# Optimization experiments

Hardware: AMD Instinct MI355X
Metric: run time of the kernel (lower is better)

## Reference

```python
import jax, jax.numpy as jnp
import numpy as np

N = 65536            # query points (256x256 image)
G = 2048             # number of gaussian/gabor primitives
K = 8                # top-k wave frequencies per primitive
NUM_TOTAL_FREQ = 128
MAX_FREQ = 128.0


def setup_inputs() -> dict:
    key = jax.random.key(0)
    ks = jax.random.split(key, 7)
    x = jax.random.uniform(ks[0], (N, 2), jnp.float32)
    gaussian_colors = 0.05 * jax.random.normal(ks[1], (G, 3), jnp.float32)
    gaussian_positions = jax.random.uniform(ks[2], (G, 2), jnp.float32)
    gaussian_scales = 3.0 + 0.05 * jax.random.normal(ks[3], (G, 2), jnp.float32)
    gaussian_rotations = jnp.pi * jax.random.uniform(ks[4], (G, 1), jnp.float32)
    topk_wave_coefficients = 0.01 * (2.0 * jax.random.uniform(ks[5], (G, K), jnp.float32) - 1.0)
    topk_wave_indices = jax.random.randint(ks[6], (G, K), 0, NUM_TOTAL_FREQ)
    return {
        "x": x,
        "gaussian_colors": gaussian_colors,
        "gaussian_positions": gaussian_positions,
        "gaussian_scales": gaussian_scales,
        "gaussian_rotations": gaussian_rotations,
        "topk_wave_coefficients": topk_wave_coefficients,
        "topk_wave_indices": topk_wave_indices,
    }


def reference(x, gaussian_colors, gaussian_positions, gaussian_scales,
              gaussian_rotations, topk_wave_coefficients, topk_wave_indices):
    # Dense (unblocked) faithful evaluation of the periodic-primitive splat:
    # out[n] = sum_g color_g * exp(-0.5*((rx*sx)^2+(ry*sy)^2)) * sum_k c_gk*cos(2*pi*f_gk*rx)
    dx = x[:, None, 0] - gaussian_positions[None, :, 0]   # [N, G]
    dy = x[:, None, 1] - gaussian_positions[None, :, 1]   # [N, G]
    th = gaussian_rotations[:, 0]                          # [G]
    c, s = jnp.cos(th), jnp.sin(th)
    rx = c[None, :] * dx + s[None, :] * dy                 # rotated coords [N, G]
    ry = -s[None, :] * dx + c[None, :] * dy
    sx = gaussian_scales[None, :, 0]
    sy = gaussian_scales[None, :, 1]
    env = jnp.exp(-0.5 * ((rx * sx) ** 2 + (ry * sy) ** 2))  # gaussian envelope [N, G]
    # frequency of each selected coefficient: idx * max_freq / num_total_freq
    freqs = topk_wave_indices.astype(jnp.float32) * (MAX_FREQ / NUM_TOTAL_FREQ)  # [G, K]
    two_pi = 2.0 * jnp.pi
    wave = jnp.zeros_like(env)
    for k in range(K):  # small fixed loop -> avoids materializing [N, G, K]
        wave = wave + topk_wave_coefficients[:, k][None, :] * jnp.cos(two_pi * freqs[:, k][None, :] * rx)
    return (env * wave) @ gaussian_colors  # [N, 3]
```

## Files before the change

kernel.cpp:

```cpp
#include <hip/hip_runtime.h>
#include <math.h>

#define G_NUM   2048
#define N_PTS   65536
#define K_FREQ  8
#define REC     64
#define CHUNKS  32
#define G_PER_CHUNK (G_NUM / CHUNKS)
#define PACK_BYTES ((size_t)G_NUM * REC * sizeof(float))
#define PART_FLOATS ((size_t)N_PTS * 3)
#define PART_BYTES_OLD (PART_FLOATS * sizeof(float) * CHUNKS)
#define LDS_FLOATS  (G_PER_CHUNK * REC)

#define S_TAB   2048
#define INV_H   (2048.0f / 3.0f)
#define TAB_BYTES   ((size_t)G_NUM * S_TAB * 16)
#define XS_BYTES    ((size_t)N_PTS * 8)
#define PERM_BYTES  ((size_t)N_PTS * 4)
#define PART4_BYTES ((size_t)CHUNKS * N_PTS * 16)
#define HIST_BYTES  ((size_t)1024 * 4)
#define OFF_TAB   (PACK_BYTES)
#define OFF_XS    (OFF_TAB + TAB_BYTES)
#define OFF_PERM  (OFF_XS + XS_BYTES)
#define OFF_PART4 (OFF_PERM + PERM_BYTES)
#define OFF_HIST  (OFF_PART4 + PART4_BYTES)
#define NEW_TOTAL (OFF_HIST + HIST_BYTES)

typedef float v2f __attribute__((ext_vector_type(2)));

#if __has_builtin(__builtin_amdgcn_cosf)
__device__ __forceinline__ float hw_cos_rev(float p) { return __builtin_amdgcn_cosf(p); }
#else
__device__ __forceinline__ float hw_cos_rev(float p) { return __cosf(6.28318530717958648f * p); }
#endif
#if __has_builtin(__builtin_amdgcn_exp2f)
__device__ __forceinline__ float hw_exp2(float p) { return __builtin_amdgcn_exp2f(p); }
#else
__device__ __forceinline__ float hw_exp2(float p) { return exp2f(p); }
#endif
#if __has_builtin(__builtin_amdgcn_fractf)
__device__ __forceinline__ float hw_fract(float p) { return __builtin_amdgcn_fractf(p); }
#else
__device__ __forceinline__ float hw_fract(float p) { return p - floorf(p); }
#endif

__device__ __forceinline__ v2f fma2v(v2f a, v2f b, v2f c) {
#if __has_builtin(__builtin_elementwise_fma)
    return __builtin_elementwise_fma(a, b, c);
#else
    v2f r; r.x = fmaf(a.x, b.x, c.x); r.y = fmaf(a.y, b.y, c.y); return r;
#endif
}

__global__ __launch_bounds__(256) void pack_kernel(
    const float* __restrict__ colors, const float* __restrict__ pos,
    const float* __restrict__ scales, const float* __restrict__ rot,
    const float* __restrict__ coef,   const int* __restrict__ idx,
    float* __restrict__ pack)
{
    int j = blockIdx.x * blockDim.x + threadIdx.x;
    if (j >= G_NUM) return;
    float th = rot[j];
    float c = cosf(th), s = sinf(th);
    float px = pos[2 * j], py = pos[2 * j + 1];
    float sx = scales[2 * j], sy = scales[2 * j + 1];
    const float nhl2e = -0.72134752044448170368f;
    float* r = pack + (size_t)j * REC;
    auto put = [&](int pair, float v) { r[2 * pair] = v; r[2 * pair + 1] = v; };
    put(0, -(c * px + s * py));
    put(1, s * px - c * py);
    put(2, c);
    put(3, s);
    put(4, -s);
    put(5, nhl2e * sx * sx);
    put(6, nhl2e * sy * sy);
    put(7, colors[3 * j]);
    put(8, colors[3 * j + 1]);
    put(9, colors[3 * j + 2]);
#pragma unroll
    for (int k = 0; k < K_FREQ; ++k) {
        put(10 + k, (float)idx[j * K_FREQ + k]);
        put(18 + k, coef[j * K_FREQ + k]);
    }
#pragma unroll
    for (int p = 26; p < 32; ++p) put(p, 0.0f);
}

template <bool USE_PART>
__global__ __launch_bounds__(256, 8) void periodic2d_kernel(
    const float* __restrict__ x, const float* __restrict__ pack,
    float* __restrict__ dst)
{
    __shared__ float lds_rec[LDS_FLOATS];
    {
        const float4* __restrict__ src = (const float4*)
            (pack + (size_t)(blockIdx.y * G_PER_CHUNK) * REC);
        float4* dstl = (float4*)lds_rec;
#pragma unroll
        for (int i = 0; i < LDS_FLOATS / 4 / 256; ++i)
            dstl[threadIdx.x + 256 * i] = src[threadIdx.x + 256 * i];
    }
    __syncthreads();

    const int t = blockIdx.x * 256 + threadIdx.x;
    const int p0 = t;
    const int p1 = t + N_PTS / 4;
    const int p2 = t + N_PTS / 2;
    const int p3 = t + 3 * (N_PTS / 4);
    const float2 q0 = ((const float2*)x)[p0];
    const float2 q1 = ((const float2*)x)[p1];
    const float2 q2 = ((const float2*)x)[p2];
    const float2 q3 = ((const float2*)x)[p3];
    const v2f xiA = {q0.x, q1.x}, yiA = {q0.y, q1.y};
    const v2f xiB = {q2.x, q3.x}, yiB = {q2.y, q3.y};
    v2f a0A = {0.f, 0.f}, a1A = {0.f, 0.f}, a2A = {0.f, 0.f};
    v2f a0B = {0.f, 0.f}, a1B = {0.f, 0.f}, a2B = {0.f, 0.f};

    const v2f* rv = (const v2f*)lds_rec;
#pragma unroll 1
    for (int j = 0; j < G_PER_CHUNK; ++j, rv += REC / 2) {
        const v2f rxA = fma2v(xiA, rv[2], fma2v(yiA, rv[3], rv[0]));
        const v2f rxB = fma2v(xiB, rv[2], fma2v(yiB, rv[3], rv[0]));
        const v2f ryA = fma2v(yiA, rv[2], fma2v(xiA, rv[4], rv[1]));
        const v2f ryB = fma2v(yiB, rv[2], fma2v(xiB, rv[4], rv[1]));
        const v2f eargA = fma2v(ryA * rv[6], ryA, (rxA * rv[5]) * rxA);
        const v2f eargB = fma2v(ryB * rv[6], ryB, (rxB * rv[5]) * rxB);
        v2f envA, envB;
        envA.x = hw_exp2(eargA.x); envA.y = hw_exp2(eargA.y);
        envB.x = hw_exp2(eargB.x); envB.y = hw_exp2(eargB.y);
        v2f waveA = {0.f, 0.f}, waveB = {0.f, 0.f};
#pragma unroll
        for (int k = 0; k < K_FREQ; ++k) {
            const v2f phA = rxA * rv[10 + k];
            const v2f phB = rxB * rv[10 + k];
            v2f cA, cB;
            cA.x = hw_cos_rev(phA.x); cA.y = hw_cos_rev(phA.y);
            cB.x = hw_cos_rev(phB.x); cB.y = hw_cos_rev(phB.y);
            waveA = fma2v(cA, rv[18 + k], waveA);
            waveB = fma2v(cB, rv[18 + k], waveB);
        }
        const v2f wA = envA * waveA;
        const v2f wB = envB * waveB;
        a0A = fma2v(wA, rv[7], a0A);  a0B = fma2v(wB, rv[7], a0B);
        a1A = fma2v(wA, rv[8], a1A);  a1B = fma2v(wB, rv[8], a1B);
        a2A = fma2v(wA, rv[9], a2A);  a2B = fma2v(wB, rv[9], a2B);
    }

    if (USE_PART) {
        float* o = dst + (size_t)blockIdx.y * PART_FLOATS;
        o[3 * p0 + 0] = a0A.x; o[3 * p0 + 1] = a1A.x; o[3 * p0 + 2] = a2A.x;
        o[3 * p1 + 0] = a0A.y; o[3 * p1 + 1] = a1A.y; o[3 * p1 + 2] = a2A.y;
        o[3 * p2 + 0] = a0B.x; o[3 * p2 + 1] = a1B.x; o[3 * p2 + 2] = a2B.x;
        o[3 * p3 + 0] = a0B.y; o[3 * p3 + 1] = a1B.y; o[3 * p3 + 2] = a2B.y;
    } else {
        atomicAdd(&dst[3 * p0 + 0], a0A.x);
        atomicAdd(&dst[3 * p0 + 1], a1A.x);
        atomicAdd(&dst[3 * p0 + 2], a2A.x);
        atomicAdd(&dst[3 * p1 + 0], a0A.y);
        atomicAdd(&dst[3 * p1 + 1], a1A.y);
        atomicAdd(&dst[3 * p1 + 2], a2A.y);
        atomicAdd(&dst[3 * p2 + 0], a0B.x);
        atomicAdd(&dst[3 * p2 + 1], a1B.x);
        atomicAdd(&dst[3 * p2 + 2], a2B.x);
        atomicAdd(&dst[3 * p3 + 0], a0B.y);
        atomicAdd(&dst[3 * p3 + 1], a1B.y);
        atomicAdd(&dst[3 * p3 + 2], a2B.y);
    }
}

__global__ __launch_bounds__(256) void reduce_kernel(
    const float* __restrict__ part, float* __restrict__ out)
{
    const int i = blockIdx.x * 256 + threadIdx.x;
    float4 s = {0.f, 0.f, 0.f, 0.f};
#pragma unroll
    for (int c = 0; c < CHUNKS; ++c) {
        const float4 v = ((const float4*)(part + (size_t)c * PART_FLOATS))[i];
        s.x += v.x; s.y += v.y; s.z += v.z; s.w += v.w;
    }
    ((float4*)out)[i] = s;
}


__global__ __launch_bounds__(256) void build_tab_kernel(
    const float* __restrict__ colors, const float* __restrict__ pos,
    const float* __restrict__ scales, const float* __restrict__ rot,
    const float* __restrict__ coef,   const int* __restrict__ idx,
    float* __restrict__ pack, float* __restrict__ tab)
{
    const int g = blockIdx.y;
    if (blockIdx.x == 0 && threadIdx.x == 0) {
        float th = rot[g];
        float c = cosf(th), s = sinf(th);
        float px = pos[2 * g], py = pos[2 * g + 1];
        float sx = scales[2 * g], sy = scales[2 * g + 1];
        const float nhl2e = -0.72134752044448170368f;
        float* r = pack + (size_t)g * REC;
        auto put = [&](int pair, float v) { r[2 * pair] = v; r[2 * pair + 1] = v; };
        put(0, -(c * px + s * py));
        put(1, s * px - c * py);
        put(2, c); put(3, s); put(4, -s);
        put(5, nhl2e * sx * sx);
        put(6, nhl2e * sy * sy);
        put(7, colors[3 * g]); put(8, colors[3 * g + 1]); put(9, colors[3 * g + 2]);
    }
    const int i = blockIdx.x * 256 + threadIdx.x;
    float nk[K_FREQ], ck[K_FREQ];
#pragma unroll
    for (int k = 0; k < K_FREQ; ++k) {
        nk[k] = (float)idx[g * K_FREQ + k];
        ck[k] = coef[g * K_FREQ + k];
    }
    float w[4];
#pragma unroll
    for (int m = 0; m < 4; ++m) {
        const float xm = (float)(3 * i + m - 3072) * 0x1p-11f;
        float acc = 0.f;
#pragma unroll
        for (int k = 0; k < K_FREQ; ++k)
            acc = fmaf(ck[k], hw_cos_rev(nk[k] * xm), acc);
        w[m] = acc;
    }
    const float d1 = w[1] - w[0];
    const float d2 = w[2] - 2.f * w[1] + w[0];
    const float d3 = w[3] - 3.f * w[2] + 3.f * w[1] - w[0];
    float4 o;
    o.x = w[0];
    o.y = 3.f * d1 - 1.5f * d2 + d3;
    o.z = 4.5f * (d2 - d3);
    o.w = 4.5f * d3;
    ((float4*)tab)[(size_t)g * S_TAB + i] = o;
}

__device__ __forceinline__ int cell_id(float px, float py) {
    int cx = (int)(px * 32.f); cx = cx > 31 ? 31 : cx;
    int cy = (int)(py * 32.f); cy = cy > 31 ? 31 : cy;
    int m = 0;
#pragma unroll
    for (int b = 0; b < 5; ++b)
        m |= (((cx >> b) & 1) << (2 * b)) | (((cy >> b) & 1) << (2 * b + 1));
    return m;
}

__global__ __launch_bounds__(256) void hist_kernel(
    const float* __restrict__ x, int* __restrict__ hist)
{
    __shared__ int h[1024];
#pragma unroll
    for (int i = 0; i < 4; ++i) h[threadIdx.x + 256 * i] = 0;
    __syncthreads();
    const int t = blockIdx.x * 256 + threadIdx.x;
    const float4 p = ((const float4*)x)[t];
    atomicAdd(&h[cell_id(p.x, p.y)], 1);
    atomicAdd(&h[cell_id(p.z, p.w)], 1);
    __syncthreads();
#pragma unroll
    for (int i = 0; i < 4; ++i) {
        const int b = threadIdx.x + 256 * i;
        const int v = h[b];
        if (v) atomicAdd(&hist[b], v);
    }
}

__global__ __launch_bounds__(1024) void scan_kernel(int* __restrict__ hist)
{
    __shared__ int e[1024];
    const int tid = threadIdx.x;
    const int v = hist[tid];
    e[tid] = v;
    __syncthreads();
#pragma unroll 1
    for (int d = 1; d < 1024; d <<= 1) {
        const int a = (tid >= d) ? e[tid - d] : 0;
        __syncthreads();
        e[tid] += a;
        __syncthreads();
    }
    hist[tid] = e[tid] - v;
}

__global__ __launch_bounds__(256) void scatter_kernel(
    const float* __restrict__ x, int* __restrict__ cursor,
    float* __restrict__ xs, int* __restrict__ perm)
{
    const int t = blockIdx.x * 256 + threadIdx.x;
    const float4 p = ((const float4*)x)[t];
    const int i0 = 2 * t;
    int pos = atomicAdd(&cursor[cell_id(p.x, p.y)], 1);
    ((float2*)xs)[pos] = make_float2(p.x, p.y);
    perm[pos] = i0;
    pos = atomicAdd(&cursor[cell_id(p.z, p.w)], 1);
    ((float2*)xs)[pos] = make_float2(p.z, p.w);
    perm[pos] = i0 + 1;
}

struct PipeSet {
    v2f envA, envB, tfA, tfB;
    float4 cA0, cA1, cB0, cB1;
    v2f col0, col1, col2;
};

__global__ __launch_bounds__(256, 4) void periodic2d_tab_kernel(
    const float* __restrict__ xs, const float* __restrict__ pack,
    const float* __restrict__ tab, float* __restrict__ part)
{
    __shared__ float lds_rec[G_PER_CHUNK * 32];
    {
        const float4* __restrict__ src = (const float4*)
            (pack + (size_t)(blockIdx.y * G_PER_CHUNK) * REC);
        float4* d4 = (float4*)lds_rec;
#pragma unroll
        for (int it = 0; it < 2; ++it) {
            const int i = threadIdx.x + 256 * it;
            d4[i] = src[((i >> 3) << 4) | (i & 7)];
        }
    }
    __syncthreads();

    const int t = blockIdx.x * 256 + threadIdx.x;
    const int p0 = ((t >> 6) << 8) | (t & 63);
    const float2 q0 = ((const float2*)xs)[p0];
    const float2 q1 = ((const float2*)xs)[p0 + 64];
    const float2 q2 = ((const float2*)xs)[p0 + 128];
    const float2 q3 = ((const float2*)xs)[p0 + 192];
    const v2f xiA = {q0.x, q1.x}, yiA = {q0.y, q1.y};
    const v2f xiB = {q2.x, q3.x}, yiB = {q2.y, q3.y};
    v2f a0A = {0.f, 0.f}, a1A = {0.f, 0.f}, a2A = {0.f, 0.f};
    v2f a0B = {0.f, 0.f}, a1B = {0.f, 0.f}, a2B = {0.f, 0.f};
    const v2f vinvh = {INV_H, INV_H};
    const v2f voff  = {1024.f, 1024.f};

    const v2f* __restrict__ rv = (const v2f*)lds_rec;
    const float4* __restrict__ tb =
        (const float4*)tab + (size_t)(blockIdx.y * G_PER_CHUNK) * S_TAB;

    PipeSet s0, s1;

    auto ISSUE = [&](PipeSet& S, const v2f* __restrict__ r,
                     const float4* __restrict__ tbl) {
        const v2f rxA = fma2v(xiA, r[2], fma2v(yiA, r[3], r[0]));
        const v2f rxB = fma2v(xiB, r[2], fma2v(yiB, r[3], r[0]));
        const v2f ryA = fma2v(yiA, r[2], fma2v(xiA, r[4], r[1]));
        const v2f ryB = fma2v(yiB, r[2], fma2v(xiB, r[4], r[1]));
        const v2f eargA = fma2v(ryA * r[6], ryA, (rxA * r[5]) * rxA);
        const v2f eargB = fma2v(ryB * r[6], ryB, (rxB * r[5]) * rxB);
        S.envA.x = hw_exp2(eargA.x); S.envA.y = hw_exp2(eargA.y);
        S.envB.x = hw_exp2(eargB.x); S.envB.y = hw_exp2(eargB.y);
        const v2f uA = fma2v(rxA, vinvh, voff);
        const v2f uB = fma2v(rxB, vinvh, voff);
        const int iA0 = (int)uA.x, iA1 = (int)uA.y;
        const int iB0 = (int)uB.x, iB1 = (int)uB.y;
        S.tfA.x = hw_fract(uA.x); S.tfA.y = hw_fract(uA.y);
        S.tfB.x = hw_fract(uB.x); S.tfB.y = hw_fract(uB.y);
        S.cA0 = tbl[iA0]; S.cA1 = tbl[iA1];
        S.cB0 = tbl[iB0]; S.cB1 = tbl[iB1];
        S.col0 = r[7]; S.col1 = r[8]; S.col2 = r[9];
    };

    auto CONSUME = [&](PipeSet& S) {
        v2f wvA, wvB;
        wvA.x = fmaf(fmaf(fmaf(S.cA0.w, S.tfA.x, S.cA0.z), S.tfA.x, S.cA0.y), S.tfA.x, S.cA0.x);
        wvA.y = fmaf(fmaf(fmaf(S.cA1.w, S.tfA.y, S.cA1.z), S.tfA.y, S.cA1.y), S.tfA.y, S.cA1.x);
        wvB.x = fmaf(fmaf(fmaf(S.cB0.w, S.tfB.x, S.cB0.z), S.tfB.x, S.cB0.y), S.tfB.x, S.cB0.x);
        wvB.y = fmaf(fmaf(fmaf(S.cB1.w, S.tfB.y, S.cB1.z), S.tfB.y, S.cB1.y), S.tfB.y, S.cB1.x);
        const v2f wA = S.envA * wvA;
        const v2f wB = S.envB * wvB;
        a0A = fma2v(wA, S.col0, a0A);  a0B = fma2v(wB, S.col0, a0B);
        a1A = fma2v(wA, S.col1, a1A);  a1B = fma2v(wB, S.col1, a1B);
        a2A = fma2v(wA, S.col2, a2A);  a2B = fma2v(wB, S.col2, a2B);
    };

    ISSUE(s0, rv,      tb);
    ISSUE(s1, rv + 16, tb + S_TAB);
#pragma unroll 1
    for (int j = 0; j < G_PER_CHUNK - 2; j += 2) {
        CONSUME(s0);
        ISSUE(s0, rv + 16 * (j + 2), tb + (size_t)S_TAB * (j + 2));
        CONSUME(s1);
        ISSUE(s1, rv + 16 * (j + 3), tb + (size_t)S_TAB * (j + 3));
    }
    CONSUME(s0);
    CONSUME(s1);

    float4* o = (float4*)part + (size_t)blockIdx.y * N_PTS;
    o[p0      ] = make_float4(a0A.x, a1A.x, a2A.x, 0.f);
    o[p0 +  64] = make_float4(a0A.y, a1A.y, a2A.y, 0.f);
    o[p0 + 128] = make_float4(a0B.x, a1B.x, a2B.x, 0.f);
    o[p0 + 192] = make_float4(a0B.y, a1B.y, a2B.y, 0.f);
}

__global__ __launch_bounds__(256) void reduce_tab_kernel(
    const float* __restrict__ part, const int* __restrict__ perm,
    float* __restrict__ out)
{
    const int p = blockIdx.x * 256 + threadIdx.x;
    const float4* p4 = (const float4*)part;
    float sx = 0.f, sy = 0.f, sz = 0.f;
#pragma unroll
    for (int c = 0; c < CHUNKS; ++c) {
        const float4 v = p4[(size_t)c * N_PTS + p];
        sx += v.x; sy += v.y; sz += v.z;
    }
    const int q = perm[p];
    out[3 * q    ] = sx;
    out[3 * q + 1] = sy;
    out[3 * q + 2] = sz;
}

extern "C" void kernel_launch(void* const* d_in, const int* in_sizes, int n_in,
                              void* d_out, int out_size, void* d_ws, size_t ws_size,
                              hipStream_t stream)
{
    const float* x      = (const float*)d_in[0];
    const float* colors = (const float*)d_in[1];
    const float* pos    = (const float*)d_in[2];
    const float* scales = (const float*)d_in[3];
    const float* rot    = (const float*)d_in[4];
    const float* coef   = (const float*)d_in[5];
    const int*   idx    = (const int*)d_in[6];
    float* out  = (float*)d_out;
    float* pack = (float*)d_ws;

    if (ws_size >= NEW_TOTAL) {
        float* tab  = (float*)((char*)d_ws + OFF_TAB);
        float* xs   = (float*)((char*)d_ws + OFF_XS);
        int*   perm = (int*)  ((char*)d_ws + OFF_PERM);
        float* part = (float*)((char*)d_ws + OFF_PART4);
        int*   hist = (int*)  ((char*)d_ws + OFF_HIST);
        (void)hipMemsetAsync(hist, 0, HIST_BYTES, stream);
        build_tab_kernel<<<dim3(S_TAB / 256, G_NUM), 256, 0, stream>>>(
            colors, pos, scales, rot, coef, idx, pack, tab);
        hist_kernel<<<dim3(N_PTS / 512), 256, 0, stream>>>(x, hist);
        scan_kernel<<<dim3(1), 1024, 0, stream>>>(hist);
        scatter_kernel<<<dim3(N_PTS / 512), 256, 0, stream>>>(x, hist, xs, perm);
        periodic2d_tab_kernel<<<dim3(N_PTS / 1024, CHUNKS), 256, 0, stream>>>(
            xs, pack, tab, part);
        reduce_tab_kernel<<<dim3(N_PTS / 256), 256, 0, stream>>>(part, perm, out);
        return;
    }

    float* part = (float*)((char*)d_ws + PACK_BYTES);
    pack_kernel<<<dim3((G_NUM + 255) / 256), 256, 0, stream>>>(
        colors, pos, scales, rot, coef, idx, pack);
    if (ws_size >= PACK_BYTES + PART_BYTES_OLD) {
        periodic2d_kernel<true><<<dim3(N_PTS / 1024, CHUNKS), 256, 0, stream>>>(
            x, pack, part);
        reduce_kernel<<<dim3((N_PTS * 3 / 4) / 256), 256, 0, stream>>>(part, out);
    } else {
        (void)hipMemsetAsync(d_out, 0, (size_t)out_size * sizeof(float), stream);
        periodic2d_kernel<false><<<dim3(N_PTS / 1024, CHUNKS), 256, 0, stream>>>(
            x, pack, out);
    }
}
```

Measured before the change: 204.2 us.

## Fuse table build with per-block histograms and drop memset and scan kernels

```diff
diff --git a/kernel.cpp b/kernel.cpp
--- a/kernel.cpp
+++ b/kernel.cpp
@@ -5,7 +5,7 @@
 #define N_PTS   65536
 #define K_FREQ  8
 #define REC     64
-#define CHUNKS  32
+#define CHUNKS  16
 #define G_PER_CHUNK (G_NUM / CHUNKS)
 #define PACK_BYTES ((size_t)G_NUM * REC * sizeof(float))
 #define PART_FLOATS ((size_t)N_PTS * 3)
@@ -14,17 +14,19 @@
 
 #define S_TAB   2048
 #define INV_H   (2048.0f / 3.0f)
+#define TAB_BLOCKS  (G_NUM * (S_TAB / 256))
+#define HIST_BLOCKS 64
 #define TAB_BYTES   ((size_t)G_NUM * S_TAB * 16)
 #define XS_BYTES    ((size_t)N_PTS * 8)
 #define PERM_BYTES  ((size_t)N_PTS * 4)
 #define PART4_BYTES ((size_t)CHUNKS * N_PTS * 16)
-#define HIST_BYTES  ((size_t)1024 * 4)
+#define PHIST_BYTES ((size_t)HIST_BLOCKS * 1024 * 4)
 #define OFF_TAB   (PACK_BYTES)
 #define OFF_XS    (OFF_TAB + TAB_BYTES)
 #define OFF_PERM  (OFF_XS + XS_BYTES)
 #define OFF_PART4 (OFF_PERM + PERM_BYTES)
-#define OFF_HIST  (OFF_PART4 + PART4_BYTES)
-#define NEW_TOTAL (OFF_HIST + HIST_BYTES)
+#define OFF_PHIST (OFF_PART4 + PART4_BYTES)
+#define NEW_TOTAL (OFF_PHIST + PHIST_BYTES)
 
 typedef float v2f __attribute__((ext_vector_type(2)));
 
@@ -182,14 +184,48 @@
 }
 
 
-__global__ __launch_bounds__(256) void build_tab_kernel(
+__device__ __forceinline__ int cell_id(float px, float py) {
+    int cx = (int)(px * 32.f); cx = cx > 31 ? 31 : cx;
+    int cy = (int)(py * 32.f); cy = cy > 31 ? 31 : cy;
+    int m = 0;
+#pragma unroll
+    for (int b = 0; b < 5; ++b)
+        m |= (((cx >> b) & 1) << (2 * b)) | (((cy >> b) & 1) << (2 * b + 1));
+    return m;
+}
+
+__global__ __launch_bounds__(256) void build_hist_kernel(
     const float* __restrict__ colors, const float* __restrict__ pos,
     const float* __restrict__ scales, const float* __restrict__ rot,
     const float* __restrict__ coef,   const int* __restrict__ idx,
-    float* __restrict__ pack, float* __restrict__ tab)
-{
-    const int g = blockIdx.y;
-    if (blockIdx.x == 0 && threadIdx.x == 0) {
+    const float* __restrict__ x,
+    float* __restrict__ pack, float* __restrict__ tab,
+    int* __restrict__ phist)
+{
+    __shared__ int h[1024];
+    const int b = blockIdx.x;
+    if (b >= TAB_BLOCKS) {
+        const int r = b - TAB_BLOCKS;
+#pragma unroll
+        for (int i = 0; i < 4; ++i) h[threadIdx.x + 256 * i] = 0;
+        __syncthreads();
+        const float4* xv = (const float4*)x + (size_t)r * 512;
+#pragma unroll
+        for (int it = 0; it < 2; ++it) {
+            const float4 p = xv[threadIdx.x + 256 * it];
+            atomicAdd(&h[cell_id(p.x, p.y)], 1);
+            atomicAdd(&h[cell_id(p.z, p.w)], 1);
+        }
+        __syncthreads();
+        int* row = phist + r * 1024;
+#pragma unroll
+        for (int i = 0; i < 4; ++i)
+            row[threadIdx.x + 256 * i] = h[threadIdx.x + 256 * i];
+        return;
+    }
+    const int g  = b >> 3;
+    const int bx = b & 7;
+    if (bx == 0 && threadIdx.x == 0) {
         float th = rot[g];
         float c = cosf(th), s = sinf(th);
         float px = pos[2 * g], py = pos[2 * g + 1];
@@ -204,7 +240,7 @@
         put(6, nhl2e * sy * sy);
         put(7, colors[3 * g]); put(8, colors[3 * g + 1]); put(9, colors[3 * g + 2]);
     }
-    const int i = blockIdx.x * 256 + threadIdx.x;
+    const int i = bx * 256 + threadIdx.x;
     float nk[K_FREQ], ck[K_FREQ];
 #pragma unroll
     for (int k = 0; k < K_FREQ; ++k) {
@@ -232,66 +268,50 @@
     ((float4*)tab)[(size_t)g * S_TAB + i] = o;
 }
 
-__device__ __forceinline__ int cell_id(float px, float py) {
-    int cx = (int)(px * 32.f); cx = cx > 31 ? 31 : cx;
-    int cy = (int)(py * 32.f); cy = cy > 31 ? 31 : cy;
-    int m = 0;
-#pragma unroll
-    for (int b = 0; b < 5; ++b)
-        m |= (((cx >> b) & 1) << (2 * b)) | (((cy >> b) & 1) << (2 * b + 1));
-    return m;
-}
-
-__global__ __launch_bounds__(256) void hist_kernel(
-    const float* __restrict__ x, int* __restrict__ hist)
-{
-    __shared__ int h[1024];
-#pragma unroll
-    for (int i = 0; i < 4; ++i) h[threadIdx.x + 256 * i] = 0;
-    __syncthreads();
-    const int t = blockIdx.x * 256 + threadIdx.x;
-    const float4 p = ((const float4*)x)[t];
-    atomicAdd(&h[cell_id(p.x, p.y)], 1);
-    atomicAdd(&h[cell_id(p.z, p.w)], 1);
-    __syncthreads();
-#pragma unroll
-    for (int i = 0; i < 4; ++i) {
-        const int b = threadIdx.x + 256 * i;
-        const int v = h[b];
-        if (v) atomicAdd(&hist[b], v);
-    }
-}
-
-__global__ __launch_bounds__(1024) void scan_kernel(int* __restrict__ hist)
-{
-    __shared__ int e[1024];
-    const int tid = threadIdx.x;
-    const int v = hist[tid];
-    e[tid] = v;
+__global__ __launch_bounds__(256) void scatter_kernel(
+    const float* __restrict__ x, const int* __restrict__ phist,
+    float* __restrict__ xs, int* __restrict__ perm)
+{
+    __shared__ int e[256];
+    __shared__ int cur[1024];
+    const int r = blockIdx.x;
+    const int t = threadIdx.x;
+    int4 tot = {0, 0, 0, 0}, base = {0, 0, 0, 0};
+#pragma unroll 1
+    for (int rr = 0; rr < HIST_BLOCKS; ++rr) {
+        const int4 v = ((const int4*)(phist + rr * 1024))[t];
+        if (rr < r) { base.x += v.x; base.y += v.y; base.z += v.z; base.w += v.w; }
+        tot.x += v.x; tot.y += v.y; tot.z += v.z; tot.w += v.w;
+    }
+    const int s4 = tot.x + tot.y + tot.z + tot.w;
+    e[t] = s4;
     __syncthreads();
 #pragma unroll 1
-    for (int d = 1; d < 1024; d <<= 1) {
-        const int a = (tid >= d) ? e[tid - d] : 0;
+    for (int d = 1; d < 256; d <<= 1) {
+        const int a = (t >= d) ? e[t - d] : 0;
         __syncthreads();
-        e[tid] += a;
+        e[t] += a;
         __syncthreads();
     }
-    hist[tid] = e[tid] - v;
-}
-
-__global__ __launch_bounds__(256) void scatter_kernel(
-    const float* __restrict__ x, int* __restrict__ cursor,
-    float* __restrict__ xs, int* __restrict__ perm)
-{
-    const int t = blockIdx.x * 256 + threadIdx.x;
-    const float4 p = ((const float4*)x)[t];
-    const int i0 = 2 * t;
-    int pos = atomicAdd(&cursor[cell_id(p.x, p.y)], 1);
-    ((float2*)xs)[pos] = make_float2(p.x, p.y);
-    perm[pos] = i0;
-    pos = atomicAdd(&cursor[cell_id(p.z, p.w)], 1);
-    ((float2*)xs)[pos] = make_float2(p.z, p.w);
-    perm[pos] = i0 + 1;
+    const int excl = e[t] - s4;
+    cur[4 * t + 0] = excl + base.x;
+    cur[4 * t + 1] = excl + tot.x + base.y;
+    cur[4 * t + 2] = excl + tot.x + tot.y + base.z;
+    cur[4 * t + 3] = excl + tot.x + tot.y + tot.z + base.w;
+    __syncthreads();
+    const float4* xv = (const float4*)x + (size_t)r * 512;
+#pragma unroll
+    for (int it = 0; it < 2; ++it) {
+        const int li = t + 256 * it;
+        const float4 p = xv[li];
+        const int i0 = 2 * (r * 512 + li);
+        int pos = atomicAdd(&cur[cell_id(p.x, p.y)], 1);
+        ((float2*)xs)[pos] = make_float2(p.x, p.y);
+        perm[pos] = i0;
+        pos = atomicAdd(&cur[cell_id(p.z, p.w)], 1);
+        ((float2*)xs)[pos] = make_float2(p.z, p.w);
+        perm[pos] = i0 + 1;
+    }
 }
 
 struct PipeSet {
@@ -310,7 +330,7 @@
             (pack + (size_t)(blockIdx.y * G_PER_CHUNK) * REC);
         float4* d4 = (float4*)lds_rec;
 #pragma unroll
-        for (int it = 0; it < 2; ++it) {
+        for (int it = 0; it < G_PER_CHUNK * 32 / 4 / 256; ++it) {
             const int i = threadIdx.x + 256 * it;
             d4[i] = src[((i >> 3) << 4) | (i & 7)];
         }
@@ -422,17 +442,14 @@
     float* pack = (float*)d_ws;
 
     if (ws_size >= NEW_TOTAL) {
-        float* tab  = (float*)((char*)d_ws + OFF_TAB);
-        float* xs   = (float*)((char*)d_ws + OFF_XS);
-        int*   perm = (int*)  ((char*)d_ws + OFF_PERM);
-        float* part = (float*)((char*)d_ws + OFF_PART4);
-        int*   hist = (int*)  ((char*)d_ws + OFF_HIST);
-        (void)hipMemsetAsync(hist, 0, HIST_BYTES, stream);
-        build_tab_kernel<<<dim3(S_TAB / 256, G_NUM), 256, 0, stream>>>(
-            colors, pos, scales, rot, coef, idx, pack, tab);
-        hist_kernel<<<dim3(N_PTS / 512), 256, 0, stream>>>(x, hist);
-        scan_kernel<<<dim3(1), 1024, 0, stream>>>(hist);
-        scatter_kernel<<<dim3(N_PTS / 512), 256, 0, stream>>>(x, hist, xs, perm);
+        float* tab   = (float*)((char*)d_ws + OFF_TAB);
+        float* xs    = (float*)((char*)d_ws + OFF_XS);
+        int*   perm  = (int*)  ((char*)d_ws + OFF_PERM);
+        float* part  = (float*)((char*)d_ws + OFF_PART4);
+        int*   phist = (int*)  ((char*)d_ws + OFF_PHIST);
+        build_hist_kernel<<<dim3(TAB_BLOCKS + HIST_BLOCKS), 256, 0, stream>>>(
+            colors, pos, scales, rot, coef, idx, x, pack, tab, phist);
+        scatter_kernel<<<dim3(HIST_BLOCKS), 256, 0, stream>>>(x, phist, xs, perm);
         periodic2d_tab_kernel<<<dim3(N_PTS / 1024, CHUNKS), 256, 0, stream>>>(
             xs, pack, tab, part);
         reduce_tab_kernel<<<dim3(N_PTS / 256), 256, 0, stream>>>(part, perm, out);
```

Measured after the change: 191.7 us. 1.07x faster.
